# Optimization experiments

Hardware: AMD Instinct MI355X
Metric: run time of the kernel (lower is better)

The kernel has to match this reference:

```python
import jax, jax.numpy as jnp
import numpy as np

STRIDE = 1
PAD = 1
EXTENT = 3  # kernel footprint (ceil of max tap offset), 3x3 tap grid


def setup_inputs() -> dict:
    key = jax.random.key(0)
    k1, k2 = jax.random.split(key)
    B, Cin, H, W = 8, 64, 128, 128
    Cout, K = 64, 9
    x = jax.random.normal(k1, (B, Cin, H, W), dtype=jnp.float32)
    # per-tap weights, one scalar weight per (out_ch, in_ch, tap) -- op formula is 'x * w'
    weights = jax.random.normal(k2, (Cout, Cin, K), dtype=jnp.float32) * 0.05
    # 3x3 integer grid shifted by +0.4 -> non-integer offsets => bilinear (sub-pixel) gather
    base = jnp.stack(jnp.meshgrid(jnp.arange(3.0), jnp.arange(3.0), indexing='ij'), -1).reshape(9, 2)
    tap_offsets = (base + 0.4).astype(jnp.float32)  # [K, 2] (dy, dx)
    return {"x": x, "weights": weights, "tap_offsets": tap_offsets}


def _bilinear_tap(xp, dy, dx, H_out, W_out):
    # Gather xp at (oy*stride + dy, ox*stride + dx) with separable bilinear interp.
    Hp, Wp = xp.shape[-2], xp.shape[-1]
    y = jnp.arange(H_out, dtype=xp.dtype) * STRIDE + dy
    xc = jnp.arange(W_out, dtype=xp.dtype) * STRIDE + dx
    y0 = jnp.floor(y)
    x0 = jnp.floor(xc)
    fy = (y - y0)[None, None, :, None]
    fx = (xc - x0)[None, None, None, :]
    y0i = jnp.clip(y0.astype(jnp.int32), 0, Hp - 1)
    y1i = jnp.clip(y0.astype(jnp.int32) + 1, 0, Hp - 1)
    x0i = jnp.clip(x0.astype(jnp.int32), 0, Wp - 1)
    x1i = jnp.clip(x0.astype(jnp.int32) + 1, 0, Wp - 1)
    # interp rows first: [B, C, H_out, Wp]
    ry = xp[:, :, y0i, :] * (1.0 - fy) + xp[:, :, y1i, :] * fy
    # then columns: [B, C, H_out, W_out]
    return ry[:, :, :, x0i] * (1.0 - fx) + ry[:, :, :, x1i] * fx


def reference(x, weights, tap_offsets):
    B, Cin, H, W = x.shape
    K = weights.shape[-1]
    xp = jnp.pad(x, ((0, 0), (0, 0), (PAD, PAD), (PAD, PAD)))
    H_out = (H + 2 * PAD - EXTENT) // STRIDE + 1
    W_out = (W + 2 * PAD - EXTENT) // STRIDE + 1
    # gather all taps (loop over small fixed K=9, each fully vectorized over B,C,H,W)
    taps = [_bilinear_tap(xp, tap_offsets[k, 0], tap_offsets[k, 1], H_out, W_out)
            for k in range(K)]
    g = jnp.stack(taps, 0)  # [K, B, Cin, H_out, W_out]
    # per-tap op 'x * w', accumulated over taps and input channels
    return jnp.einsum('kbiyx,oik->boyx', g, weights)  # [B, Cout, H_out, W_out]
```

## Files before the change

### kernel.cpp

```cpp
#include <hip/hip_runtime.h>


#define CIN   64
#define COUT  64
#define HH    128
#define WW    128
#define NC    68

typedef __attribute__((ext_vector_type(8))) short bf16x8;
typedef __attribute__((ext_vector_type(4))) float f32x4;
typedef __attribute__((ext_vector_type(4))) unsigned int u32x4;

__device__ __forceinline__ unsigned short f2bf(float f) {
  unsigned int u = __float_as_uint(f);
  u = (u + 0x7fffu + ((u >> 16) & 1u)) >> 16;
  return (unsigned short)u;
}

__device__ __forceinline__ unsigned int cvtpk(float lo, float hi) {
  unsigned int r;
  asm("v_cvt_pk_bf16_f32 %0, %1, %2" : "=v"(r) : "v"(lo), "v"(hi));
  return r;
}

__global__ void make_wb(const float* __restrict__ wgt,
                        const float* __restrict__ off,
                        unsigned short* __restrict__ wb2)
{
  int id = blockIdx.x * 64 + threadIdx.x;
  int o = id >> 6, c = id & 63;
  float W16[16];
  #pragma unroll
  for (int i = 0; i < 16; ++i) W16[i] = 0.f;
  for (int k = 0; k < 9; ++k) {
    float dy = off[2*k], dx = off[2*k+1];
    float fyf = floorf(dy), fxf = floorf(dx);
    int   iy = (int)fyf,   ix = (int)fxf;
    float fy = dy - fyf,   fx = dx - fxf;
    float wk = wgt[(o*CIN + c)*9 + k];
    W16[(iy  )*4 + ix  ] += wk * (1.f-fy)*(1.f-fx);
    W16[(iy  )*4 + ix+1] += wk * (1.f-fy)*fx;
    W16[(iy+1)*4 + ix  ] += wk * fy*(1.f-fx);
    W16[(iy+1)*4 + ix+1] += wk * fy*fx;
  }
  int p = c >> 5, q = (c >> 3) & 3, j = c & 7;
  int n = o >> 4, m15 = o & 15;
  int lanei = q*16 + m15;
  for (int rs = 0; rs < 16; ++rs)
    wb2[(size_t)(((p*16 + rs)*4 + n)*64 + lanei)*8 + j] = f2bf(W16[rs]);
}

__global__ __launch_bounds__(128, 4)
void conv_mfma(const float* __restrict__ x,
               const unsigned short* __restrict__ wb2,
               float* __restrict__ out)
{
  __shared__ __align__(16) unsigned short tile[4 * NC * 32];

  const int wg  = blockIdx.x;
  const int xcd = wg & 7;
  const int i   = wg >> 3;
  const int b   = i >> 5;
  const int r5  = i & 31;
  const int y0  = xcd * 16 + (r5 >> 1);
  const int x0  = (r5 & 1) * 64;
  const int t    = threadIdx.x;
  const int wave = t >> 6;
  const int lane = t & 63;
  const int m15  = lane & 15;
  const int q    = lane >> 4;
  const int wv   = __builtin_amdgcn_readfirstlane(wave);

  int gx   = x0 - 1 + lane;
  bool gxv = ((unsigned)gx < (unsigned)WW);
  int gxc  = gx < 0 ? 0 : (gx > WW-1 ? WW-1 : gx);
  int gxh  = x0 + 63 + lane;
  bool gxhv = ((unsigned)gxh < (unsigned)WW);
  int gxhc = gxh < 0 ? 0 : (gxh > WW-1 ? WW-1 : gxh);

  const int w4 = (lane >> 2) & 3;
  char* pst[2];
  pst[0] = (char*)tile + lane*64 + ((wv     + w4) & 3)*16;
  pst[1] = (char*)tile + lane*64 + ((wv + 2 + w4) & 3)*16;

  const char* aptr[4];
  #pragma unroll
  for (int s = 0; s < 4; ++s) {
    int c0   = m15 + s;
    int slot = (q + (c0 >> 2)) & 3;
    aptr[s] = (const char*)tile + c0*64 + slot*16;
  }

  f32x4 acc[4][2];
  #pragma unroll
  for (int mi = 0; mi < 4; ++mi)
    #pragma unroll
    for (int nn = 0; nn < 2; ++nn)
      acc[mi][nn] = (f32x4){0.f, 0.f, 0.f, 0.f};

  #pragma unroll
  for (int p = 0; p < 2; ++p) {
    if (p) __syncthreads();

    #pragma unroll
    for (int it = 0; it < 8; ++it) {
      const int row   = it >> 1;
      const int j     = it & 1;
      const int chunk = wv + 2*j;
      const int gy    = y0 + row - 1;
      char* dst = pst[j] + row*4352;
      if ((unsigned)gy < (unsigned)HH) {
        const float* ps = x + ((size_t)((b*CIN + p*32 + chunk*8)*HH + gy))*WW;
        float v[8];
        #pragma unroll
        for (int cc = 0; cc < 8; ++cc) v[cc] = ps[(size_t)cc*HH*WW + gxc];
        unsigned int pk[4];
        #pragma unroll
        for (int ii = 0; ii < 4; ++ii) {
          pk[ii] = cvtpk(v[2*ii], v[2*ii+1]);
          pk[ii] = gxv ? pk[ii] : 0u;
        }
        *(u32x4*)dst = *(u32x4*)pk;
        if (lane < 3) {
          float vh[8];
          #pragma unroll
          for (int cc = 0; cc < 8; ++cc) vh[cc] = ps[(size_t)cc*HH*WW + gxhc];
          unsigned int ph[4];
          #pragma unroll
          for (int ii = 0; ii < 4; ++ii) {
            ph[ii] = cvtpk(vh[2*ii], vh[2*ii+1]);
            ph[ii] = gxhv ? ph[ii] : 0u;
          }
          *(u32x4*)(dst + 4096) = *(u32x4*)ph;
        }
      } else if (p == 0) {
        *(u32x4*)dst = (u32x4){0u,0u,0u,0u};
        if (lane < 3) *(u32x4*)(dst + 4096) = (u32x4){0u,0u,0u,0u};
      }
    }
    __syncthreads();

    const char* wp = (const char*)wb2 + (size_t)p*65536 + wave*2048 + (size_t)lane*16;
    #pragma unroll
    for (int rs = 0; rs < 16; ++rs) {
      const int r = rs >> 2, s = rs & 3;
      bf16x8 bfr[2];
      bfr[0] = *(const bf16x8*)(wp + rs*4096);
      bfr[1] = *(const bf16x8*)(wp + rs*4096 + 1024);
      bf16x8 afr[4];
      #pragma unroll
      for (int mi = 0; mi < 4; ++mi)
        afr[mi] = *(const bf16x8*)(aptr[s] + r*4352 + mi*1024);
      #pragma unroll
      for (int mi = 0; mi < 4; ++mi)
        #pragma unroll
        for (int nn = 0; nn < 2; ++nn)
          acc[mi][nn] = __builtin_amdgcn_mfma_f32_16x16x32_bf16(afr[mi], bfr[nn], acc[mi][nn], 0, 0, 0);
    }
  }

  __syncthreads();
  float* epi = (float*)tile;
  #pragma unroll
  for (int mi = 0; mi < 4; ++mi)
    #pragma unroll
    for (int nn = 0; nn < 2; ++nn) {
      int o  = (wave*2 + nn)*16 + m15;
      int px = mi*16 + q*4;
      *(f32x4*)&epi[o*NC + px] = acc[mi][nn];
    }
  __syncthreads();
  #pragma unroll
  for (int round = 0; round < 8; ++round) {
    int idx = round*512 + t*4;
    int o = idx >> 6, px = idx & 63;
    f32x4 v = *(const f32x4*)&epi[o*NC + px];
    *(f32x4*)&out[(((size_t)(b*COUT + o))*HH + y0)*WW + x0 + px] = v;
  }
}

extern "C" void kernel_launch(void* const* d_in, const int* in_sizes, int n_in,
                              void* d_out, int out_size, void* d_ws, size_t ws_size,
                              hipStream_t stream)
{
  const float* x   = (const float*)d_in[0];
  const float* wgt = (const float*)d_in[1];
  const float* off = (const float*)d_in[2];
  float* out = (float*)d_out;
  unsigned short* wb2 = (unsigned short*)d_ws;

  make_wb<<<64, 64, 0, stream>>>(wgt, off, wb2);
  conv_mfma<<<2048, 128, 0, stream>>>(x, wb2, out);
}
```

Baseline: 107.1 us.

## Use four waves per block, one output-channel tile each, and store directly

```diff
diff --git a/kernel.cpp b/kernel.cpp
--- a/kernel.cpp
+++ b/kernel.cpp
@@ -50,7 +50,7 @@
     wb2[(size_t)(((p*16 + rs)*4 + n)*64 + lanei)*8 + j] = f2bf(W16[rs]);
 }
 
-__global__ __launch_bounds__(128, 4)
+__global__ __launch_bounds__(256, 8)
 void conv_mfma(const float* __restrict__ x,
                const unsigned short* __restrict__ wb2,
                float* __restrict__ out)
@@ -79,9 +79,7 @@
   int gxhc = gxh < 0 ? 0 : (gxh > WW-1 ? WW-1 : gxh);
 
   const int w4 = (lane >> 2) & 3;
-  char* pst[2];
-  pst[0] = (char*)tile + lane*64 + ((wv     + w4) & 3)*16;
-  pst[1] = (char*)tile + lane*64 + ((wv + 2 + w4) & 3)*16;
+  char* pst = (char*)tile + lane*64 + ((wv + w4) & 3)*16;
 
   const char* aptr[4];
   #pragma unroll
@@ -91,26 +89,21 @@
     aptr[s] = (const char*)tile + c0*64 + slot*16;
   }
 
-  f32x4 acc[4][2];
+  f32x4 acc[4];
   #pragma unroll
   for (int mi = 0; mi < 4; ++mi)
-    #pragma unroll
-    for (int nn = 0; nn < 2; ++nn)
-      acc[mi][nn] = (f32x4){0.f, 0.f, 0.f, 0.f};
+    acc[mi] = (f32x4){0.f, 0.f, 0.f, 0.f};
 
   #pragma unroll
   for (int p = 0; p < 2; ++p) {
     if (p) __syncthreads();
 
     #pragma unroll
-    for (int it = 0; it < 8; ++it) {
-      const int row   = it >> 1;
-      const int j     = it & 1;
-      const int chunk = wv + 2*j;
-      const int gy    = y0 + row - 1;
-      char* dst = pst[j] + row*4352;
+    for (int it = 0; it < 4; ++it) {
+      const int gy = y0 + it - 1;
+      char* dst = pst + it*4352;
       if ((unsigned)gy < (unsigned)HH) {
-        const float* ps = x + ((size_t)((b*CIN + p*32 + chunk*8)*HH + gy))*WW;
+        const float* ps = x + ((size_t)((b*CIN + p*32 + wv*8)*HH + gy))*WW;
         float v[8];
         #pragma unroll
         for (int cc = 0; cc < 8; ++cc) v[cc] = ps[(size_t)cc*HH*WW + gxc];
@@ -140,43 +133,28 @@
     }
     __syncthreads();
 
-    const char* wp = (const char*)wb2 + (size_t)p*65536 + wave*2048 + (size_t)lane*16;
+    const char* wp = (const char*)wb2 + (size_t)p*65536 + wv*1024 + (size_t)lane*16;
+    __builtin_amdgcn_s_setprio(1);
     #pragma unroll
     for (int rs = 0; rs < 16; ++rs) {
       const int r = rs >> 2, s = rs & 3;
-      bf16x8 bfr[2];
-      bfr[0] = *(const bf16x8*)(wp + rs*4096);
-      bfr[1] = *(const bf16x8*)(wp + rs*4096 + 1024);
+      bf16x8 bfr = *(const bf16x8*)(wp + rs*4096);
       bf16x8 afr[4];
       #pragma unroll
       for (int mi = 0; mi < 4; ++mi)
         afr[mi] = *(const bf16x8*)(aptr[s] + r*4352 + mi*1024);
       #pragma unroll
       for (int mi = 0; mi < 4; ++mi)
-        #pragma unroll
-        for (int nn = 0; nn < 2; ++nn)
-          acc[mi][nn] = __builtin_amdgcn_mfma_f32_16x16x32_bf16(afr[mi], bfr[nn], acc[mi][nn], 0, 0, 0);
+        acc[mi] = __builtin_amdgcn_mfma_f32_16x16x32_bf16(afr[mi], bfr, acc[mi], 0, 0, 0);
     }
+    __builtin_amdgcn_s_setprio(0);
   }
 
-  __syncthreads();
-  float* epi = (float*)tile;
+  const int o = wave*16 + m15;
+  float* orow = out + (((size_t)(b*COUT + o))*HH + y0)*WW + x0 + q*4;
   #pragma unroll
   for (int mi = 0; mi < 4; ++mi)
-    #pragma unroll
-    for (int nn = 0; nn < 2; ++nn) {
-      int o  = (wave*2 + nn)*16 + m15;
-      int px = mi*16 + q*4;
-      *(f32x4*)&epi[o*NC + px] = acc[mi][nn];
-    }
-  __syncthreads();
-  #pragma unroll
-  for (int round = 0; round < 8; ++round) {
-    int idx = round*512 + t*4;
-    int o = idx >> 6, px = idx & 63;
-    f32x4 v = *(const f32x4*)&epi[o*NC + px];
-    *(f32x4*)&out[(((size_t)(b*COUT + o))*HH + y0)*WW + x0 + px] = v;
-  }
+    *(f32x4*)&orow[mi*16] = acc[mi];
 }
 
 extern "C" void kernel_launch(void* const* d_in, const int* in_sizes, int n_in,
@@ -190,5 +168,5 @@
   unsigned short* wb2 = (unsigned short*)d_ws;
 
   make_wb<<<64, 64, 0, stream>>>(wgt, off, wb2);
-  conv_mfma<<<2048, 128, 0, stream>>>(x, wb2, out);
+  conv_mfma<<<2048, 256, 0, stream>>>(x, wb2, out);
 }
```

New measurement: 109.7 us. 2.4% more time.
